# Performance work log

Measured on AMD Instinct MI355X. Metric: run time of the kernel, lower is better.

Reference implementation:

```python
import jax, jax.numpy as jnp
import numpy as np

H, D_MODEL, LEN_Q, LEN_K, D_K, D_V = 16, 1024, 2048, 2048, 64, 64
BATCH = 4
SCALE = 1.0 / np.sqrt(float(D_K))


def setup_inputs() -> dict:
    key = jax.random.key(0)
    ks = jax.random.split(key, 10)
    inp = {
        "Q": jax.random.normal(ks[0], (BATCH, LEN_Q, D_MODEL), dtype=jnp.float32),
        "K": jax.random.normal(ks[1], (BATCH, LEN_K, D_MODEL), dtype=jnp.float32),
        "V": jax.random.normal(ks[2], (BATCH, LEN_K, D_MODEL), dtype=jnp.float32),
        "mask": jax.random.randint(ks[3], (BATCH, LEN_K), 0, 2, dtype=jnp.int32),
        # Linear params (torch Linear: y = x @ W.T + b); store W as [in, out].
        "Wq": jax.random.normal(ks[4], (D_MODEL, H * D_K), dtype=jnp.float32) * (1.0 / np.sqrt(D_MODEL)),
        "bq": jnp.zeros((H * D_K,), dtype=jnp.float32),
        "Wk": jax.random.normal(ks[5], (D_MODEL, H * D_K), dtype=jnp.float32) * (1.0 / np.sqrt(D_MODEL)),
        "bk": jnp.zeros((H * D_K,), dtype=jnp.float32),
        "Wv": jax.random.normal(ks[6], (D_MODEL, H * D_V), dtype=jnp.float32) * (1.0 / np.sqrt(D_MODEL)),
        "bv": jnp.zeros((H * D_V,), dtype=jnp.float32),
    }
    return inp


def reference(Q, K, V, mask, Wq, bq, Wk, bk, Wv, bv):
    B = Q.shape[0]
    # Projections -> [B, S, H, d]
    q = (Q @ Wq + bq).reshape(B, LEN_Q, H, D_K)
    k = (K @ Wk + bk).reshape(B, LEN_K, H, D_K)
    v = (V @ Wv + bv).reshape(B, LEN_K, H, D_V)
    # Scores: [B, H, len_q, len_k]
    scores = jnp.einsum("bqhd,bkhd->bhqk", q, k) * SCALE
    # Key-padding mask broadcast over heads and queries
    scores = jnp.where(mask[:, None, None, :] == 0, jnp.float32(-1e9), scores)
    alpha = jax.nn.softmax(scores, axis=-1)
    out = jnp.einsum("bhqk,bkhd->bqhd", alpha, v)  # [B, len_q, H, d_v]
    return out.reshape(B, LEN_Q, H * D_V)
```

## Files before the change

kernel.cpp:

```cpp
#include <hip/hip_runtime.h>

#define NH 16
#define DM 1024
#define SQ 2048
#define BT 4

typedef __attribute__((ext_vector_type(8))) short bf16x8;
typedef __attribute__((ext_vector_type(4))) short sh4;
typedef __attribute__((ext_vector_type(4))) float f4;
typedef __attribute__((ext_vector_type(4))) float fv4;
typedef unsigned short u16;

#define M2BIAS 23.083120654f
#define SCALE2 0.18033688f

__device__ __forceinline__ u16 f2bf(float f) {
    union { float f; unsigned u; } v; v.f = f;
    unsigned r = v.u + 0x7FFFu + ((v.u >> 16) & 1u);
    return (u16)(r >> 16);
}

__device__ __forceinline__ float fast_exp2(float x) {
#if __has_builtin(__builtin_amdgcn_exp2f)
    return __builtin_amdgcn_exp2f(x);
#else
    return exp2f(x);
#endif
}

#if __has_builtin(__builtin_amdgcn_mfma_f32_16x16x16_bf16)
#define MFMA16(a, b, c) __builtin_amdgcn_mfma_f32_16x16x16_bf16(a, b, c, 0, 0, 0)
#elif __has_builtin(__builtin_amdgcn_mfma_f32_16x16x16bf16_1k)
#define MFMA16(a, b, c) __builtin_amdgcn_mfma_f32_16x16x16bf16_1k(a, b, c, 0, 0, 0)
#else
static __device__ __forceinline__ f4 mfma16_asm(sh4 a, sh4 b, f4 c) {
    asm("v_mfma_f32_16x16x16_bf16 %0, %1, %2, %0" : "+v"(c) : "v"(a), "v"(b));
    return c;
}
#define MFMA16(a, b, c) mfma16_asm(a, b, c)
#endif

#define GLD16(gp, lp) __builtin_amdgcn_global_load_lds( \
    (const __attribute__((address_space(1))) void*)(gp), \
    (__attribute__((address_space(3))) void*)(lp), 16, 0, 0)

__global__ __launch_bounds__(256) void cvt_x(const float* __restrict__ x, u16* __restrict__ y) {
    int i = blockIdx.x * 256 + threadIdx.x;
    fv4 v = ((const fv4*)x)[i];
    sh4 r;
    r[0] = (short)f2bf(v[0]); r[1] = (short)f2bf(v[1]);
    r[2] = (short)f2bf(v[2]); r[3] = (short)f2bf(v[3]);
    ((sh4*)y)[i] = r;
}

__global__ __launch_bounds__(256) void cvt_wT(const float* __restrict__ Wsrc, u16* __restrict__ Wt) {
    __shared__ float t[64][65];
    int r0 = blockIdx.x * 64, c0 = blockIdx.y * 64;
    #pragma unroll
    for (int i = 0; i < 16; ++i) {
        int idx = i * 256 + threadIdx.x;
        int r = idx >> 6, c = idx & 63;
        t[r][c] = Wsrc[(size_t)(r0 + r) * DM + c0 + c];
    }
    __syncthreads();
    #pragma unroll
    for (int i = 0; i < 16; ++i) {
        int idx = i * 256 + threadIdx.x;
        int n = idx >> 6, k = idx & 63;
        Wt[(size_t)(c0 + n) * DM + r0 + k] = f2bf(t[k][n]);
    }
}

__global__ __launch_bounds__(256) void mk_mbias(const int* __restrict__ mask, float* __restrict__ mb) {
    int i = blockIdx.x * 256 + threadIdx.x;
    mb[i] = mask[i] ? -M2BIAS : -__builtin_inff();
}

__global__ __launch_bounds__(256) void gemm_proj(const u16* __restrict__ A, const u16* __restrict__ Bt,
                                                 const float* __restrict__ bias, u16* __restrict__ outp,
                                                 int vmode) {
    __shared__ u16 As[128 * 64];
    __shared__ u16 Bs[128 * 64];
    int tid = threadIdx.x;
    int w = tid >> 6, lane = tid & 63, quad = lane >> 4, l16 = lane & 15;
    int wm = w >> 1, wn = w & 1;
    int r8 = lane >> 3, cg = (lane & 7) ^ r8;
    const u16* Ag = A + (size_t)blockIdx.x * 128 * DM;
    const u16* Bg = Bt + (size_t)blockIdx.y * 128 * DM;

    f4 acc[4][4];
    #pragma unroll
    for (int mt = 0; mt < 4; ++mt)
        #pragma unroll
        for (int nt = 0; nt < 4; ++nt) acc[mt][nt] = f4{0.f, 0.f, 0.f, 0.f};

    for (int kt = 0; kt < 16; ++kt) {
        int kofs = kt * 64 + cg * 8;
        #pragma unroll
        for (int c = 0; c < 4; ++c) {
            int rbase = w * 32 + c * 8;
            GLD16(Ag + (size_t)(rbase + r8) * DM + kofs, &As[rbase * 64]);
            GLD16(Bg + (size_t)(rbase + r8) * DM + kofs, &Bs[rbase * 64]);
        }
        __syncthreads();
        #pragma unroll
        for (int ks = 0; ks < 2; ++ks) {
            bf16x8 afr[4], bfr[4];
            #pragma unroll
            for (int mt = 0; mt < 4; ++mt) {
                int row = wm * 64 + mt * 16 + l16;
                int ch = (ks * 4 + quad) ^ (row & 7);
                afr[mt] = *(const bf16x8*)&As[row * 64 + ch * 8];
            }
            #pragma unroll
            for (int nt = 0; nt < 4; ++nt) {
                int row = wn * 64 + nt * 16 + l16;
                int ch = (ks * 4 + quad) ^ (row & 7);
                bfr[nt] = *(const bf16x8*)&Bs[row * 64 + ch * 8];
            }
            #pragma unroll
            for (int mt = 0; mt < 4; ++mt)
                #pragma unroll
                for (int nt = 0; nt < 4; ++nt)
                    acc[mt][nt] = __builtin_amdgcn_mfma_f32_16x16x32_bf16(afr[mt], bfr[nt], acc[mt][nt], 0, 0, 0);
        }
        __syncthreads();
    }

    #pragma unroll
    for (int nt = 0; nt < 4; ++nt) {
        int ncol = blockIdx.y * 128 + wn * 64 + nt * 16 + l16;
        float bn = bias[ncol];
        int h = ncol >> 6, d = ncol & 63;
        #pragma unroll
        for (int mt = 0; mt < 4; ++mt) {
            int mbase = blockIdx.x * 128 + wm * 64 + mt * 16 + quad * 4;
            int bidx = mbase >> 11, s0 = mbase & 2047;
            if (vmode == 0) {
                size_t base = ((size_t)bidx * NH + h) * SQ;
                #pragma unroll
                for (int reg = 0; reg < 4; ++reg)
                    outp[(base + s0 + reg) * 64 + d] = f2bf(acc[mt][nt][reg] + bn);
            } else {
                sh4 pk;
                #pragma unroll
                for (int reg = 0; reg < 4; ++reg) pk[reg] = (short)f2bf(acc[mt][nt][reg] + bn);
                *(sh4*)&outp[(((size_t)bidx * NH + h) * 64 + d) * SQ + s0] = pk;
            }
        }
    }
}

__global__ __launch_bounds__(256, 4) void attn(const u16* __restrict__ qw, const u16* __restrict__ kw,
                                               const u16* __restrict__ vtw, const float* __restrict__ mbias,
                                               float* __restrict__ outp) {
    __shared__ u16 Ks[2][64 * 64];
    __shared__ u16 Vs[2][64 * 64];
    int tid = threadIdx.x;
    int w = tid >> 6, lane = tid & 63, quad = lane >> 4, l16 = lane & 15;
    int r8 = lane >> 3, sl = lane & 7;
    int bh = blockIdx.x, b = bh >> 4;
    int h = bh & 15;
    int qbase = blockIdx.y * 128 + w * 32;
    const u16* qp = qw + (size_t)bh * SQ * 64;
    const u16* kp = kw + (size_t)bh * SQ * 64;
    const u16* vp = vtw + (size_t)bh * 64 * SQ;
    const float* mbp = mbias + b * SQ;

    bf16x8 aq[2][2];
    #pragma unroll
    for (int mt = 0; mt < 2; ++mt)
        #pragma unroll
        for (int ks = 0; ks < 2; ++ks)
            aq[mt][ks] = *(const bf16x8*)&qp[(size_t)(qbase + mt * 16 + l16) * 64 + ks * 32 + quad * 8];

    f4 o[2][4];
    float lrow[2] = {0.f, 0.f};
    #pragma unroll
    for (int mt = 0; mt < 2; ++mt)
        #pragma unroll
        for (int nt = 0; nt < 4; ++nt) o[mt][nt] = f4{0.f, 0.f, 0.f, 0.f};

    auto stage = [&](int buf, int k0) {
        #pragma unroll
        for (int j = 0; j < 2; ++j) {
            int row = w * 16 + j * 8 + r8;
            int gsl = sl ^ (row & 7);
            GLD16(kp + (size_t)(k0 + row) * 64 + gsl * 8, &Ks[buf][(w * 16 + j * 8) * 64]);
            GLD16(vp + (size_t)row * SQ + k0 + gsl * 8, &Vs[buf][(w * 16 + j * 8) * 64]);
        }
    };

    stage(0, 0);
    for (int kb = 0; kb < 32; ++kb) {
        int buf = kb & 1;
        int k0 = kb * 64;
        __syncthreads();
        fv4 bias4[4];
        #pragma unroll
        for (int kt = 0; kt < 4; ++kt)
            bias4[kt] = *(const fv4*)&mbp[k0 + kt * 16 + quad * 4];
        if (kb + 1 < 32) stage(buf ^ 1, k0 + 64);

        bf16x8 bk[4][2];
        #pragma unroll
        for (int kt = 0; kt < 4; ++kt)
            #pragma unroll
            for (int ks = 0; ks < 2; ++ks) {
                int r = kt * 16 + l16;
                int slot = (ks * 4 + quad) ^ (r & 7);
                bk[kt][ks] = *(const bf16x8*)&Ks[buf][r * 64 + slot * 8];
            }
        f4 S[4][2];
        #pragma unroll
        for (int kt = 0; kt < 4; ++kt)
            #pragma unroll
            for (int mt = 0; mt < 2; ++mt) {
                f4 s = f4{0.f, 0.f, 0.f, 0.f};
                s = __builtin_amdgcn_mfma_f32_16x16x32_bf16(bk[kt][0], aq[mt][0], s, 0, 0, 0);
                s = __builtin_amdgcn_mfma_f32_16x16x32_bf16(bk[kt][1], aq[mt][1], s, 0, 0, 0);
                S[kt][mt] = s;
            }
        #pragma unroll
        for (int kt = 0; kt < 4; ++kt) {
            sh4 pa[2];
            #pragma unroll
            for (int mt = 0; mt < 2; ++mt) {
                f4 s = S[kt][mt];
                float p0 = fast_exp2(s[0] * SCALE2 + bias4[kt][0]);
                float p1 = fast_exp2(s[1] * SCALE2 + bias4[kt][1]);
                float p2 = fast_exp2(s[2] * SCALE2 + bias4[kt][2]);
                float p3 = fast_exp2(s[3] * SCALE2 + bias4[kt][3]);
                lrow[mt] += (p0 + p1) + (p2 + p3);
                pa[mt][0] = (short)(__float_as_uint(p0) >> 16);
                pa[mt][1] = (short)(__float_as_uint(p1) >> 16);
                pa[mt][2] = (short)(__float_as_uint(p2) >> 16);
                pa[mt][3] = (short)(__float_as_uint(p3) >> 16);
            }
            sh4 bv[4];
            #pragma unroll
            for (int nt = 0; nt < 4; ++nt) {
                int row = nt * 16 + l16;
                int ch = (2 * kt + (quad >> 1)) ^ (row & 7);
                bv[nt] = *(const sh4*)&Vs[buf][row * 64 + ch * 8 + (quad & 1) * 4];
            }
            #pragma unroll
            for (int mt = 0; mt < 2; ++mt)
                #pragma unroll
                for (int nt = 0; nt < 4; ++nt)
                    o[mt][nt] = MFMA16(pa[mt], bv[nt], o[mt][nt]);
        }
    }

    #pragma unroll
    for (int mt = 0; mt < 2; ++mt) {
        float v = lrow[mt];
        v += __shfl_xor(v, 16);
        v += __shfl_xor(v, 32);
        #pragma unroll
        for (int reg = 0; reg < 4; ++reg) {
            float inv = 1.f / __shfl(v, quad * 4 + reg);
            int row = qbase + mt * 16 + quad * 4 + reg;
            size_t obase = ((size_t)b * SQ + row) * DM + h * 64;
            #pragma unroll
            for (int nt = 0; nt < 4; ++nt)
                outp[obase + nt * 16 + l16] = o[mt][nt][reg] * inv;
        }
    }
}

extern "C" void kernel_launch(void* const* d_in, const int* in_sizes, int n_in,
                              void* d_out, int out_size, void* d_ws, size_t ws_size,
                              hipStream_t stream) {
    (void)in_sizes; (void)n_in; (void)out_size; (void)ws_size;
    const float* Q  = (const float*)d_in[0];
    const float* K  = (const float*)d_in[1];
    const float* V  = (const float*)d_in[2];
    const int* mask = (const int*)d_in[3];
    const float* Wq = (const float*)d_in[4];
    const float* bq = (const float*)d_in[5];
    const float* Wk = (const float*)d_in[6];
    const float* bk = (const float*)d_in[7];
    const float* Wv = (const float*)d_in[8];
    const float* bv = (const float*)d_in[9];
    float* out = (float*)d_out;
    char* ws = (char*)d_ws;
    u16* q_ws = (u16*)(ws);
    u16* k_ws = (u16*)(ws + (size_t)16 * 1024 * 1024);
    u16* v_ws = (u16*)(ws + (size_t)32 * 1024 * 1024);
    u16* xbuf = (u16*)(ws + (size_t)48 * 1024 * 1024);
    u16* wbuf = (u16*)(ws + (size_t)64 * 1024 * 1024);
    float* mb = (float*)(ws + (size_t)48 * 1024 * 1024);

    dim3 gGemm(64, 8), gW(16, 16);
    cvt_x<<<8192, 256, 0, stream>>>(Q, xbuf);
    cvt_wT<<<gW, 256, 0, stream>>>(Wq, wbuf);
    gemm_proj<<<gGemm, 256, 0, stream>>>(xbuf, wbuf, bq, q_ws, 0);
    cvt_x<<<8192, 256, 0, stream>>>(K, xbuf);
    cvt_wT<<<gW, 256, 0, stream>>>(Wk, wbuf);
    gemm_proj<<<gGemm, 256, 0, stream>>>(xbuf, wbuf, bk, k_ws, 0);
    cvt_x<<<8192, 256, 0, stream>>>(V, xbuf);
    cvt_wT<<<gW, 256, 0, stream>>>(Wv, wbuf);
    gemm_proj<<<gGemm, 256, 0, stream>>>(xbuf, wbuf, bv, v_ws, 1);
    mk_mbias<<<32, 256, 0, stream>>>(mask, mb);
    attn<<<dim3(64, 16), 256, 0, stream>>>(q_ws, k_ws, v_ws, mb, out);
}
```

Measured before the change: 339.2 us.

## Use 16x16x32 MFMA for PV by permuting key order in K and mask

Replaces the PV product's 16x16x16 bf16 MFMAs with 16x16x32 MFMAs, which halves the instruction count and lets V be read from shared memory as 8-element vectors. To make the score accumulator layout match the K=32 operand layout without shuffles, keys are permuted within 32-key groups when K is written by the projection GEMM and when the mask bias is built. P is then packed from pairs of score tiles. This adds register pressure from holding all the P values at once and relies on the permutation being applied consistently everywhere keys are indexed.

```diff
diff --git a/kernel.cpp b/kernel.cpp
--- a/kernel.cpp
+++ b/kernel.cpp
@@ -28,17 +28,9 @@
 #endif
 }
 
-#if __has_builtin(__builtin_amdgcn_mfma_f32_16x16x16_bf16)
-#define MFMA16(a, b, c) __builtin_amdgcn_mfma_f32_16x16x16_bf16(a, b, c, 0, 0, 0)
-#elif __has_builtin(__builtin_amdgcn_mfma_f32_16x16x16bf16_1k)
-#define MFMA16(a, b, c) __builtin_amdgcn_mfma_f32_16x16x16bf16_1k(a, b, c, 0, 0, 0)
-#else
-static __device__ __forceinline__ f4 mfma16_asm(sh4 a, sh4 b, f4 c) {
-    asm("v_mfma_f32_16x16x16_bf16 %0, %1, %2, %0" : "+v"(c) : "v"(a), "v"(b));
-    return c;
-}
-#define MFMA16(a, b, c) mfma16_asm(a, b, c)
-#endif
+__device__ __forceinline__ int prem(int s) {
+    return (s & ~31) | ((s & 4) << 2) | ((s >> 1) & 12) | (s & 3);
+}
 
 #define GLD16(gp, lp) __builtin_amdgcn_global_load_lds( \
     (const __attribute__((address_space(1))) void*)(gp), \
@@ -73,7 +65,7 @@
 
 __global__ __launch_bounds__(256) void mk_mbias(const int* __restrict__ mask, float* __restrict__ mb) {
     int i = blockIdx.x * 256 + threadIdx.x;
-    mb[i] = mask[i] ? -M2BIAS : -__builtin_inff();
+    mb[prem(i)] = mask[i] ? -M2BIAS : -__builtin_inff();
 }
 
 __global__ __launch_bounds__(256) void gemm_proj(const u16* __restrict__ A, const u16* __restrict__ Bt,
@@ -136,16 +128,17 @@
         for (int mt = 0; mt < 4; ++mt) {
             int mbase = blockIdx.x * 128 + wm * 64 + mt * 16 + quad * 4;
             int bidx = mbase >> 11, s0 = mbase & 2047;
-            if (vmode == 0) {
-                size_t base = ((size_t)bidx * NH + h) * SQ;
-                #pragma unroll
-                for (int reg = 0; reg < 4; ++reg)
-                    outp[(base + s0 + reg) * 64 + d] = f2bf(acc[mt][nt][reg] + bn);
-            } else {
+            if (vmode == 1) {
                 sh4 pk;
                 #pragma unroll
                 for (int reg = 0; reg < 4; ++reg) pk[reg] = (short)f2bf(acc[mt][nt][reg] + bn);
                 *(sh4*)&outp[(((size_t)bidx * NH + h) * 64 + d) * SQ + s0] = pk;
+            } else {
+                int sp = (vmode == 2) ? prem(s0) : s0;
+                size_t base = ((size_t)bidx * NH + h) * SQ;
+                #pragma unroll
+                for (int reg = 0; reg < 4; ++reg)
+                    outp[(base + sp + reg) * 64 + d] = f2bf(acc[mt][nt][reg] + bn);
             }
         }
     }
@@ -222,33 +215,44 @@
                 S[kt][mt] = s;
             }
         #pragma unroll
-        for (int kt = 0; kt < 4; ++kt) {
-            sh4 pa[2];
+        for (int kt = 0; kt < 4; ++kt)
             #pragma unroll
             for (int mt = 0; mt < 2; ++mt) {
                 f4 s = S[kt][mt];
-                float p0 = fast_exp2(s[0] * SCALE2 + bias4[kt][0]);
-                float p1 = fast_exp2(s[1] * SCALE2 + bias4[kt][1]);
-                float p2 = fast_exp2(s[2] * SCALE2 + bias4[kt][2]);
-                float p3 = fast_exp2(s[3] * SCALE2 + bias4[kt][3]);
-                lrow[mt] += (p0 + p1) + (p2 + p3);
-                pa[mt][0] = (short)(__float_as_uint(p0) >> 16);
-                pa[mt][1] = (short)(__float_as_uint(p1) >> 16);
-                pa[mt][2] = (short)(__float_as_uint(p2) >> 16);
-                pa[mt][3] = (short)(__float_as_uint(p3) >> 16);
-            }
-            sh4 bv[4];
+                f4 p;
+                p[0] = fast_exp2(s[0] * SCALE2 + bias4[kt][0]);
+                p[1] = fast_exp2(s[1] * SCALE2 + bias4[kt][1]);
+                p[2] = fast_exp2(s[2] * SCALE2 + bias4[kt][2]);
+                p[3] = fast_exp2(s[3] * SCALE2 + bias4[kt][3]);
+                lrow[mt] += (p[0] + p[1]) + (p[2] + p[3]);
+                S[kt][mt] = p;
+            }
+        #pragma unroll
+        for (int g = 0; g < 2; ++g) {
+            bf16x8 pa8[2];
+            #pragma unroll
+            for (int mt = 0; mt < 2; ++mt) {
+                f4 pe = S[2 * g][mt], po = S[2 * g + 1][mt];
+                unsigned w0 = (__float_as_uint(pe[1]) & 0xFFFF0000u) | (__float_as_uint(pe[0]) >> 16);
+                unsigned w1 = (__float_as_uint(pe[3]) & 0xFFFF0000u) | (__float_as_uint(pe[2]) >> 16);
+                unsigned w2 = (__float_as_uint(po[1]) & 0xFFFF0000u) | (__float_as_uint(po[0]) >> 16);
+                unsigned w3 = (__float_as_uint(po[3]) & 0xFFFF0000u) | (__float_as_uint(po[2]) >> 16);
+                union { unsigned u[4]; bf16x8 v; } cv;
+                cv.u[0] = w0; cv.u[1] = w1; cv.u[2] = w2; cv.u[3] = w3;
+                pa8[mt] = cv.v;
+            }
+            bf16x8 bv8[4];
             #pragma unroll
             for (int nt = 0; nt < 4; ++nt) {
                 int row = nt * 16 + l16;
-                int ch = (2 * kt + (quad >> 1)) ^ (row & 7);
-                bv[nt] = *(const sh4*)&Vs[buf][row * 64 + ch * 8 + (quad & 1) * 4];
+                int ch = (g * 4 + quad) ^ (row & 7);
+                bv8[nt] = *(const bf16x8*)&Vs[buf][row * 64 + ch * 8];
             }
             #pragma unroll
             for (int mt = 0; mt < 2; ++mt)
                 #pragma unroll
                 for (int nt = 0; nt < 4; ++nt)
-                    o[mt][nt] = MFMA16(pa[mt], bv[nt], o[mt][nt]);
+                    o[mt][nt] = __builtin_amdgcn_mfma_f32_16x16x32_bf16(pa8[mt], bv8[nt], o[mt][nt], 0, 0, 0);
         }
     }
 
@@ -298,7 +302,7 @@
     gemm_proj<<<gGemm, 256, 0, stream>>>(xbuf, wbuf, bq, q_ws, 0);
     cvt_x<<<8192, 256, 0, stream>>>(K, xbuf);
     cvt_wT<<<gW, 256, 0, stream>>>(Wk, wbuf);
-    gemm_proj<<<gGemm, 256, 0, stream>>>(xbuf, wbuf, bk, k_ws, 0);
+    gemm_proj<<<gGemm, 256, 0, stream>>>(xbuf, wbuf, bk, k_ws, 2);
     cvt_x<<<8192, 256, 0, stream>>>(V, xbuf);
     cvt_wT<<<gW, 256, 0, stream>>>(Wv, wbuf);
     gemm_proj<<<gGemm, 256, 0, stream>>>(xbuf, wbuf, bv, v_ws, 1);
```

Measured after the change: 393.7 us. 16.1% more time.
